# Kernel tuning notes

Measured on AMD Instinct MI355X. Metric: run time of the kernel, lower is better.

Reference implementation:

```python
import jax, jax.numpy as jnp
import numpy as np

C, C_H, N_HEAD = 256, 32, 8
LN_EPS = 1e-5


def setup_inputs() -> dict:
    key = jax.random.key(0)
    ks = jax.random.split(key, 10)
    B, S, I = 1, 256, 384
    hc = C_H * N_HEAD
    w = lambda k, shp: (jax.random.normal(k, shp, dtype=jnp.float32) * 0.02)
    return {
        "m": jax.random.normal(ks[0], (B, S, I, C), dtype=jnp.float32),
        "msa_mask": jnp.ones((B, S, I), dtype=jnp.float32),
        "gamma": jnp.ones((C,), dtype=jnp.float32),
        "beta": jnp.zeros((C,), dtype=jnp.float32),
        "Wq": w(ks[1], (C, hc)),
        "Wk": w(ks[2], (C, hc)),
        "Wv": w(ks[3], (C, hc)),
        "Wg": w(ks[4], (C, hc)),
        "bg": jnp.zeros((hc,), dtype=jnp.float32),
        "Wo": w(ks[5], (hc, C)),
        "bo": jnp.zeros((C,), dtype=jnp.float32),
    }


def reference(m, msa_mask, gamma, beta, Wq, Wk, Wv, Wg, bg, Wo, bo):
    B, S, I, _ = m.shape
    h, ch = N_HEAD, C_H
    # LayerNorm over channel dim
    mu = jnp.mean(m, axis=-1, keepdims=True)
    var = jnp.mean((m - mu) ** 2, axis=-1, keepdims=True)
    x = (m - mu) * jax.lax.rsqrt(var + LN_EPS) * gamma + beta  # (B,s,i,c)
    # projections -> (B,s,i,h,ch)
    q = (x @ Wq).reshape(B, S, I, h, ch)
    k = (x @ Wk).reshape(B, S, I, h, ch)
    v = (x @ Wv).reshape(B, S, I, h, ch)
    gate = jax.nn.sigmoid(x @ Wg + bg).reshape(B, S, I, h, ch)
    # column-wise attention over s, per column i and head h
    a = jnp.einsum("bsihc,btihc->bihst", q, k) / np.float32(np.sqrt(ch))
    # additive mask bias: msa_mask (B,s,i) -> (B,i,s) -> (B,i,1,1,s)
    bias = (1e9 * (jnp.swapaxes(msa_mask, -1, -2) - 1.0))[:, :, None, None, :]
    a = jax.nn.softmax(a + bias, axis=-1)
    # weighted values -> (B,s,i,h,ch)
    o = jnp.einsum("bihst,btihc->bsihc", a, v)
    o = (gate * o).reshape(B, S, I, h * ch)
    return o @ Wo + bo
```

## Files before the change

kernel.cpp:

```cpp
#include <hip/hip_runtime.h>

typedef unsigned short ushort_t;
typedef __attribute__((ext_vector_type(4))) short short4v;
typedef __attribute__((ext_vector_type(8))) short short8;
typedef __attribute__((ext_vector_type(4))) float floatx4;

#define SEQ 256
#define NI 384
#define CDIM 256
#define NH 8
#define CH 32
#define HC 256
#define NROW (SEQ * NI)
#define QKVG_N 1024

__device__ __forceinline__ float b2f(ushort_t u) {
  union { unsigned int i; float f; } z;
  z.i = ((unsigned int)u) << 16;
  return z.f;
}
__device__ __forceinline__ ushort_t f2b(float f) {
  union { float f; unsigned int i; } z;
  z.f = f;
  unsigned int x = z.i;
  unsigned int r = (x + 0x7fffu + ((x >> 16) & 1u)) >> 16;
  return (ushort_t)r;
}
__device__ __forceinline__ unsigned int pkbf16(float a, float b) {
  union { float f; unsigned int i; } za, zb;
  za.f = a; zb.f = b;
  unsigned int ra = za.i + 0x7fffu + ((za.i >> 16) & 1u);
  unsigned int rb = zb.i + 0x7fffu + ((zb.i >> 16) & 1u);
  return __builtin_amdgcn_perm(rb, ra, 0x07060302u);
}
__device__ __forceinline__ float ldx(const void* p, size_t i, int f32) {
  if (f32) return ((const float*)p)[i];
  return b2f(((const ushort_t*)p)[i]);
}
__device__ __forceinline__ short8 mk8(unsigned int a, unsigned int b, unsigned int c,
                                      unsigned int d) {
  union { unsigned int u[4]; short8 s; } z;
  z.u[0] = a; z.u[1] = b; z.u[2] = c; z.u[3] = d;
  return z.s;
}

__global__ void detect_kernel(const unsigned int* __restrict__ g, int* __restrict__ flag) {
  *flag = (g[0] == 0x3F800000u) ? 1 : 0;
}

__global__ __launch_bounds__(256) void ln_norm_kernel(
    const void* __restrict__ m, const void* __restrict__ gamma, const void* __restrict__ beta,
    const int* __restrict__ pflag, ushort_t* __restrict__ xln) {
  int f32 = *pflag;
  int wave = threadIdx.x >> 6, lane = threadIdx.x & 63;
  int row = blockIdx.x * 4 + wave;
  size_t base = (size_t)row * CDIM + lane * 4;
  float v[4], g[4], b[4];
  if (f32) {
    floatx4 vv = *(const floatx4*)((const float*)m + base);
    floatx4 gg = *(const floatx4*)((const float*)gamma + lane * 4);
    floatx4 bb = *(const floatx4*)((const float*)beta + lane * 4);
    #pragma unroll
    for (int j = 0; j < 4; ++j) { v[j] = vv[j]; g[j] = gg[j]; b[j] = bb[j]; }
  } else {
    short4v vv = *(const short4v*)((const ushort_t*)m + base);
    short4v gg = *(const short4v*)((const ushort_t*)gamma + lane * 4);
    short4v bb = *(const short4v*)((const ushort_t*)beta + lane * 4);
    #pragma unroll
    for (int j = 0; j < 4; ++j) {
      v[j] = b2f((ushort_t)vv[j]); g[j] = b2f((ushort_t)gg[j]); b[j] = b2f((ushort_t)bb[j]);
    }
  }
  float s1 = 0.f, s2 = 0.f;
  #pragma unroll
  for (int j = 0; j < 4; ++j) { s1 += v[j]; s2 += v[j] * v[j]; }
  #pragma unroll
  for (int off = 1; off < 64; off <<= 1) {
    s1 += __shfl_xor(s1, off);
    s2 += __shfl_xor(s2, off);
  }
  float mu = s1 * (1.0f / CDIM);
  float var = s2 * (1.0f / CDIM) - mu * mu;
  float rstd = rsqrtf(var + 1e-5f);
  short4v o;
  #pragma unroll
  for (int j = 0; j < 4; ++j) o[j] = (short)f2b((v[j] - mu) * rstd * g[j] + b[j]);
  *(short4v*)(xln + base) = o;
}

__global__ void transpose5(const void* a0, const void* a1, const void* a2, const void* a3,
                           const void* a4, const int* __restrict__ pflag,
                           ushort_t* __restrict__ Wqkvg, ushort_t* __restrict__ WoT) {
  int f32 = *pflag;
  int z = blockIdx.z;
  const void* src = (z == 0) ? a0 : (z == 1) ? a1 : (z == 2) ? a2 : (z == 3) ? a3 : a4;
  int x = blockIdx.x * 16 + threadIdx.x;
  int y = blockIdx.y * 16 + threadIdx.y;
  ushort_t val = f2b(ldx(src, (size_t)y * 256 + x, f32));
  if (z < 4) Wqkvg[((size_t)z * 256 + x) * 256 + y] = val;
  else       WoT[(size_t)x * 256 + y] = val;
}

#define LDT 56

__global__ __launch_bounds__(256) void gemm128(
    const ushort_t* __restrict__ A, const ushort_t* __restrict__ Bt,
    void* __restrict__ C, const void* __restrict__ bias, const int* __restrict__ pflag,
    int N, int epi, int CW, int i0, int mapA, int mapC) {
  int flag = *pflag;
  __shared__ __align__(16) ushort_t lA[128 * LDT];
  __shared__ __align__(16) ushort_t lB[128 * LDT];
  int tid = threadIdx.x;
  int m0 = blockIdx.x * 128, n0 = blockIdx.y * 128;
  int wave = tid >> 6, lane = tid & 63, lr = lane & 15, lq = lane >> 4;
  int wr = wave >> 1, wc = wave & 1;

  floatx4 acc[4][4];
  #pragma unroll
  for (int a = 0; a < 4; ++a)
    #pragma unroll
    for (int b = 0; b < 4; ++b) {
      acc[a][b][0] = 0.f; acc[a][b][1] = 0.f; acc[a][b][2] = 0.f; acc[a][b][3] = 0.f;
    }

  int row = tid >> 1, koff = (tid & 1) * 16;
  int rloc = m0 + row;
  int growA = mapA ? ((rloc / CW) * NI + i0 + (rloc % CW)) : rloc;
  const ushort_t* Ap = A + (size_t)growA * CDIM + koff;
  const ushort_t* Bp = Bt + (size_t)(n0 + row) * CDIM + koff;

  for (int k0 = 0; k0 < CDIM; k0 += 32) {
    short8 a0 = *(const short8*)(Ap + k0);
    short8 a1 = *(const short8*)(Ap + k0 + 8);
    short8 b0 = *(const short8*)(Bp + k0);
    short8 b1 = *(const short8*)(Bp + k0 + 8);
    *(short8*)&lA[row * LDT + koff] = a0;
    *(short8*)&lA[row * LDT + koff + 8] = a1;
    *(short8*)&lB[row * LDT + koff] = b0;
    *(short8*)&lB[row * LDT + koff + 8] = b1;
    __syncthreads();
    short8 af[4], bf[4];
    #pragma unroll
    for (int jm = 0; jm < 4; ++jm)
      af[jm] = *(const short8*)&lA[(wr * 64 + jm * 16 + lr) * LDT + lq * 8];
    #pragma unroll
    for (int jn = 0; jn < 4; ++jn)
      bf[jn] = *(const short8*)&lB[(wc * 64 + jn * 16 + lr) * LDT + lq * 8];
    #pragma unroll
    for (int jm = 0; jm < 4; ++jm)
      #pragma unroll
      for (int jn = 0; jn < 4; ++jn)
        acc[jm][jn] = __builtin_amdgcn_mfma_f32_16x16x32_bf16(af[jm], bf[jn], acc[jm][jn], 0, 0, 0);
    __syncthreads();
  }

  #pragma unroll
  for (int jm = 0; jm < 4; ++jm) {
    #pragma unroll
    for (int jn = 0; jn < 4; ++jn) {
      int col = n0 + wc * 64 + jn * 16 + lr;
      #pragma unroll
      for (int r = 0; r < 4; ++r) {
        int rl = m0 + wr * 64 + jm * 16 + lq * 4 + r;
        float val = acc[jm][jn][r];
        if (epi == 1) {
          if (col >= 768) {
            val += ldx(bias, col - 768, flag);
            val = 1.0f / (1.0f + __expf(-val));
          }
          ((ushort_t*)C)[(size_t)rl * N + col] = f2b(val);
        } else {
          val += ldx(bias, col, flag);
          int g = mapC ? ((rl / CW) * NI + i0 + (rl % CW)) : rl;
          if (flag) ((float*)C)[(size_t)g * N + col] = val;
          else      ((ushort_t*)C)[(size_t)g * N + col] = f2b(val);
        }
      }
    }
  }
}

#define KSTR 40
#define VSTR 264

__global__ __launch_bounds__(256) void attn_mfma(
    const ushort_t* __restrict__ qkvg, const void* __restrict__ mask,
    const int* __restrict__ pflag, ushort_t* __restrict__ xln, int CW, int i0) {
  int f32 = *pflag;
  int il = blockIdx.x, h = blockIdx.y;
  __shared__ __align__(16) ushort_t Kl[SEQ * KSTR];
  __shared__ __align__(16) ushort_t Vt[CH * VSTR];
  __shared__ __align__(16) float biasS[SEQ];
  int tid = threadIdx.x;

  {
    int t = tid;
    size_t base = ((size_t)t * CW + il) * QKVG_N + h * CH;
    short8 kv[4], vv[4];
    #pragma unroll
    for (int c4 = 0; c4 < 4; ++c4) {
      kv[c4] = *(const short8*)(qkvg + base + 256 + c4 * 8);
      vv[c4] = *(const short8*)(qkvg + base + 512 + c4 * 8);
    }
    #pragma unroll
    for (int c4 = 0; c4 < 4; ++c4) *(short8*)&Kl[t * KSTR + c4 * 8] = kv[c4];
    int kpos = 32 * (t >> 5) + 8 * ((t >> 2) & 3) + 4 * ((t >> 4) & 1) + (t & 3);
    #pragma unroll
    for (int c4 = 0; c4 < 4; ++c4)
      #pragma unroll
      for (int j = 0; j < 8; ++j)
        Vt[(c4 * 8 + j) * VSTR + kpos] = (ushort_t)vv[c4][j];
    biasS[t] = 1e9f * (ldx(mask, (size_t)t * NI + i0 + il, f32) - 1.0f);
  }
  __syncthreads();

  int wave = tid >> 6, lane = tid & 63, lr = lane & 15, quad = lane >> 4;
  const float scale = 0.17677669529663687f;

  short8 qf = *(const short8*)(qkvg +
      ((size_t)(wave * 64 + lr) * CW + il) * QKVG_N + h * CH + quad * 8);

  #pragma unroll 1
  for (int mt = 0; mt < 4; ++mt) {
    int sbase = wave * 64 + mt * 16;
    float m_run = -3.0e38f, l_run = 0.f;
    floatx4 o0, o1;
    o0[0] = 0.f; o0[1] = 0.f; o0[2] = 0.f; o0[3] = 0.f;
    o1 = o0;
    short8 qfn;
    float g0[4], g1[4];

    #pragma unroll 1
    for (int half = 0; half < 2; ++half) {
      floatx4 s[8];
      #pragma unroll
      for (int tt = 0; tt < 8; ++tt) {
        short8 kb = *(const short8*)&Kl[((half * 8 + tt) * 16 + lr) * KSTR + quad * 8];
        floatx4 z;
        z[0] = 0.f; z[1] = 0.f; z[2] = 0.f; z[3] = 0.f;
        s[tt] = __builtin_amdgcn_mfma_f32_16x16x32_bf16(kb, qf, z, 0, 0, 0);
      }

      if (half == 0) {
        int nmt = (mt + 1) & 3;
        qfn = *(const short8*)(qkvg +
            ((size_t)(wave * 64 + nmt * 16 + lr) * CW + il) * QKVG_N + h * CH + quad * 8);
        #pragma unroll
        for (int r = 0; r < 4; ++r) {
          size_t gbase =
              ((size_t)(sbase + quad * 4 + r) * CW + il) * QKVG_N + 768 + h * CH;
          g0[r] = b2f(qkvg[gbase + lr]);
          g1[r] = b2f(qkvg[gbase + 16 + lr]);
        }
      }

      float mx0 = -3.0e38f, mx1 = -3.0e38f, mx2 = -3.0e38f, mx3 = -3.0e38f;
      #pragma unroll
      for (int tt = 0; tt < 8; ++tt) {
        floatx4 bb = *(const floatx4*)&biasS[(half * 8 + tt) * 16 + quad * 4];
        s[tt][0] = s[tt][0] * scale + bb[0];
        s[tt][1] = s[tt][1] * scale + bb[1];
        s[tt][2] = s[tt][2] * scale + bb[2];
        s[tt][3] = s[tt][3] * scale + bb[3];
        mx0 = fmaxf(mx0, s[tt][0]);
        mx1 = fmaxf(mx1, s[tt][1]);
        mx2 = fmaxf(mx2, s[tt][2]);
        mx3 = fmaxf(mx3, s[tt][3]);
      }
      float mh = fmaxf(fmaxf(mx0, mx1), fmaxf(mx2, mx3));
      mh = fmaxf(mh, __shfl_xor(mh, 16));
      mh = fmaxf(mh, __shfl_xor(mh, 32));
      float mnew = fmaxf(m_run, mh);
      float fsc = __expf(m_run - mnew);

      float su0 = 0.f, su1 = 0.f, su2 = 0.f, su3 = 0.f;
      #pragma unroll
      for (int tt = 0; tt < 8; ++tt) {
        s[tt][0] = __expf(s[tt][0] - mnew);
        s[tt][1] = __expf(s[tt][1] - mnew);
        s[tt][2] = __expf(s[tt][2] - mnew);
        s[tt][3] = __expf(s[tt][3] - mnew);
        su0 += s[tt][0];
        su1 += s[tt][1];
        su2 += s[tt][2];
        su3 += s[tt][3];
      }
      float lh = (su0 + su1) + (su2 + su3);
      lh += __shfl_xor(lh, 16);
      lh += __shfl_xor(lh, 32);
      l_run = l_run * fsc + lh;
      m_run = mnew;

      unsigned int p2[8][2];
      #pragma unroll
      for (int tt = 0; tt < 8; ++tt) {
        p2[tt][0] = pkbf16(s[tt][0], s[tt][1]);
        p2[tt][1] = pkbf16(s[tt][2], s[tt][3]);
      }

      #pragma unroll
      for (int r = 0; r < 4; ++r) {
        float fr = __shfl(fsc, quad * 4 + r);
        o0[r] *= fr;
        o1[r] *= fr;
      }
      #pragma unroll
      for (int tc = 0; tc < 4; ++tc) {
        short8 af = mk8(p2[2 * tc][0], p2[2 * tc][1], p2[2 * tc + 1][0], p2[2 * tc + 1][1]);
        short8 v0 = *(const short8*)&Vt[lr * VSTR + (half * 4 + tc) * 32 + quad * 8];
        short8 v1 =
            *(const short8*)&Vt[(16 + lr) * VSTR + (half * 4 + tc) * 32 + quad * 8];
        o0 = __builtin_amdgcn_mfma_f32_16x16x32_bf16(af, v0, o0, 0, 0, 0);
        o1 = __builtin_amdgcn_mfma_f32_16x16x32_bf16(af, v1, o1, 0, 0, 0);
      }
    }

    float inv = 1.0f / l_run;
    #pragma unroll
    for (int r = 0; r < 4; ++r) {
      float invr = __shfl(inv, quad * 4 + r);
      int srow = sbase + quad * 4 + r;
      size_t grow = (size_t)srow * NI + i0 + il;
      xln[grow * HC + h * CH + lr] = f2b(o0[r] * invr * g0[r]);
      xln[grow * HC + h * CH + 16 + lr] = f2b(o1[r] * invr * g1[r]);
    }
    qf = qfn;
  }
}

extern "C" void kernel_launch(void* const* d_in, const int* in_sizes, int n_in,
                              void* d_out, int out_size, void* d_ws, size_t ws_size,
                              hipStream_t stream) {
  const void* m     = d_in[0];
  const void* mask  = d_in[1];
  const void* gamma = d_in[2];
  const void* beta  = d_in[3];
  const void* Wq    = d_in[4];
  const void* Wk    = d_in[5];
  const void* Wv    = d_in[6];
  const void* Wg    = d_in[7];
  const void* bg    = d_in[8];
  const void* Wo    = d_in[9];
  const void* bo    = d_in[10];

  auto need = [](int nc) -> size_t {
    return 4096 + (size_t)QKVG_N * 256 * 2 + 256 * 256 * 2 + (size_t)NROW * CDIM * 2 +
           (size_t)SEQ * (NI / nc) * QKVG_N * 2 + 4096;
  };
  int nch = 1;
  while (nch < 8 && need(nch) > ws_size) nch *= 2;
  int CW = NI / nch;

  char* ws = (char*)d_ws;
  size_t off = 0;
  auto alloc = [&](size_t bytes) -> void* {
    void* p = ws + off;
    off += (bytes + 255) & ~(size_t)255;
    return p;
  };
  int* pflag       = (int*)alloc(256);
  ushort_t* WqkvgT = (ushort_t*)alloc((size_t)QKVG_N * 256 * 2);
  ushort_t* WoT    = (ushort_t*)alloc(256 * 256 * 2);
  ushort_t* xln    = (ushort_t*)alloc((size_t)NROW * CDIM * 2);
  ushort_t* qkvg   = (ushort_t*)alloc((size_t)SEQ * CW * QKVG_N * 2);

  detect_kernel<<<1, 1, 0, stream>>>((const unsigned int*)gamma, pflag);
  ln_norm_kernel<<<NROW / 4, 256, 0, stream>>>(m, gamma, beta, pflag, xln);
  transpose5<<<dim3(16, 16, 5), dim3(16, 16), 0, stream>>>(Wq, Wk, Wv, Wg, Wo, pflag,
                                                           WqkvgT, WoT);
  for (int c = 0; c < nch; ++c) {
    int i0 = c * CW;
    int M = SEQ * CW;
    gemm128<<<dim3(M / 128, QKVG_N / 128), 256, 0, stream>>>(
        xln, WqkvgT, qkvg, bg, pflag, QKVG_N, 1, CW, i0, 1, 0);
    attn_mfma<<<dim3(CW, NH), 256, 0, stream>>>(qkvg, mask, pflag, xln, CW, i0);
    gemm128<<<dim3(M / 128, CDIM / 128), 256, 0, stream>>>(
        xln, WoT, d_out, bo, pflag, CDIM, 2, CW, i0, 1, 1);
  }
}
```

Measured before the change: 478.4 us.

## Prefetch next K-tile into registers and remap GEMM blocks across XCDs

```diff
diff --git a/kernel.cpp b/kernel.cpp
--- a/kernel.cpp
+++ b/kernel.cpp
@@ -106,12 +106,18 @@
 __global__ __launch_bounds__(256) void gemm128(
     const ushort_t* __restrict__ A, const ushort_t* __restrict__ Bt,
     void* __restrict__ C, const void* __restrict__ bias, const int* __restrict__ pflag,
-    int N, int epi, int CW, int i0, int mapA, int mapC) {
+    int N, int epi, int CW, int i0, int mapA, int mapC, int nN) {
   int flag = *pflag;
   __shared__ __align__(16) ushort_t lA[128 * LDT];
   __shared__ __align__(16) ushort_t lB[128 * LDT];
   int tid = threadIdx.x;
-  int m0 = blockIdx.x * 128, n0 = blockIdx.y * 128;
+
+  int nblk = gridDim.x;
+  int bid = blockIdx.x;
+  int lin = (bid & 7) * (nblk >> 3) + (bid >> 3);
+  int mb = lin / nN, nb = lin - mb * nN;
+  int m0 = mb * 128, n0 = nb * 128;
+
   int wave = tid >> 6, lane = tid & 63, lr = lane & 15, lq = lane >> 4;
   int wr = wave >> 1, wc = wave & 1;
 
@@ -129,15 +135,23 @@
   const ushort_t* Ap = A + (size_t)growA * CDIM + koff;
   const ushort_t* Bp = Bt + (size_t)(n0 + row) * CDIM + koff;
 
+  short8 a0 = *(const short8*)(Ap);
+  short8 a1 = *(const short8*)(Ap + 8);
+  short8 b0 = *(const short8*)(Bp);
+  short8 b1 = *(const short8*)(Bp + 8);
+
+  #pragma unroll 1
   for (int k0 = 0; k0 < CDIM; k0 += 32) {
-    short8 a0 = *(const short8*)(Ap + k0);
-    short8 a1 = *(const short8*)(Ap + k0 + 8);
-    short8 b0 = *(const short8*)(Bp + k0);
-    short8 b1 = *(const short8*)(Bp + k0 + 8);
     *(short8*)&lA[row * LDT + koff] = a0;
     *(short8*)&lA[row * LDT + koff + 8] = a1;
     *(short8*)&lB[row * LDT + koff] = b0;
     *(short8*)&lB[row * LDT + koff + 8] = b1;
+    if (k0 + 32 < CDIM) {
+      a0 = *(const short8*)(Ap + k0 + 32);
+      a1 = *(const short8*)(Ap + k0 + 40);
+      b0 = *(const short8*)(Bp + k0 + 32);
+      b1 = *(const short8*)(Bp + k0 + 40);
+    }
     __syncthreads();
     short8 af[4], bf[4];
     #pragma unroll
@@ -371,10 +385,10 @@
   for (int c = 0; c < nch; ++c) {
     int i0 = c * CW;
     int M = SEQ * CW;
-    gemm128<<<dim3(M / 128, QKVG_N / 128), 256, 0, stream>>>(
-        xln, WqkvgT, qkvg, bg, pflag, QKVG_N, 1, CW, i0, 1, 0);
+    gemm128<<<(M / 128) * (QKVG_N / 128), 256, 0, stream>>>(
+        xln, WqkvgT, qkvg, bg, pflag, QKVG_N, 1, CW, i0, 1, 0, QKVG_N / 128);
     attn_mfma<<<dim3(CW, NH), 256, 0, stream>>>(qkvg, mask, pflag, xln, CW, i0);
-    gemm128<<<dim3(M / 128, CDIM / 128), 256, 0, stream>>>(
-        xln, WoT, d_out, bo, pflag, CDIM, 2, CW, i0, 1, 1);
-  }
-}
+    gemm128<<<(M / 128) * (CDIM / 128), 256, 0, stream>>>(
+        xln, WoT, d_out, bo, pflag, CDIM, 2, CW, i0, 1, 1, CDIM / 128);
+  }
+}
```

After: 524.4 us. 1.1x slower.
